# Optimization experiments

Measured on AMD Instinct MI355X. Metric: run time of the kernel, lower is better.

The kernel has to match this reference:

```python
import jax, jax.numpy as jnp
import numpy as np

N = 2048        # nodes
IN_DIM = 128    # input feature dim
K = 8           # channels
D = 32          # per-channel dim (C_dim)
ITERS = 4       # routing iterations
BETA = 1.0      # attention temperature
EPS = 1e-12     # F.normalize eps


def l2norm(x):
    # F.normalize(x, dim=-1): x / max(||x||_2, eps)
    n = jnp.linalg.norm(x, axis=-1, keepdims=True)
    return x / jnp.maximum(n, EPS)


def setup_inputs() -> dict:
    key = jax.random.key(0)
    k1, k2, k3, k4 = jax.random.split(key, 4)
    adj = jax.random.randint(k1, (N, N), 0, 2, dtype=jnp.int32)
    features = jax.random.normal(k2, (N, IN_DIM), dtype=jnp.float32)
    # parameters initialized ~ N(0,1) as in init_parameters
    W = jax.random.normal(k3, (K, IN_DIM, D), dtype=jnp.float32)
    b = jax.random.normal(k4, (K, D), dtype=jnp.float32)
    return {"adj": adj, "features": features, "W": W, "b": b}


def reference(adj, features, W, b):
    mask = (adj > 0)[None, :, :]                         # [1, N, N]
    # per-channel projection + row L2 normalize -> Z: [K, N, D]
    Z = l2norm(jnp.einsum('nd,kdc->knc', features, W) + b[:, None, :])
    for _ in range(ITERS):
        # per-channel masked attention scores [K, N, N]
        att = jnp.einsum('knc,kmc->knm', Z, Z)
        att = jnp.where(mask, att, 0.0) / BETA
        # softmax across channels (dim=2 in torch after cat == K axis here)
        att = jax.nn.softmax(att, axis=0)
        att = jnp.where(mask, att, 0.0)
        # weighted aggregate + residual + L2 normalize
        Z = l2norm(Z + jnp.einsum('knm,kmc->knc', att, Z))
    # concat channels along feature dim -> [N, K*D]
    return jnp.transpose(Z, (1, 0, 2)).reshape(N, K * D)
```

## Files before the change

kernel.cpp:

```cpp
#include <hip/hip_runtime.h>
#include <hip/hip_bf16.h>

#define NN 2048
#define KK 8
#define DD 32
#define ZSZ (KK * NN * DD)

typedef __attribute__((ext_vector_type(8))) short short8;
typedef __attribute__((ext_vector_type(4))) float f32x4;
typedef __attribute__((ext_vector_type(4))) unsigned int u32x4;

union UU { u32x4 q; short8 v; unsigned int u[4]; };

#define SELHI 0x07060302u
#define SELLO 0x05040100u
#define PSTR 20

__device__ __forceinline__ unsigned int prm(unsigned int a, unsigned int b, unsigned int sel) {
  return __builtin_amdgcn_perm(a, b, sel);
}
__device__ __forceinline__ unsigned int bfr(float x) {
  unsigned int u = __float_as_uint(x);
  return (u + 0x7fffu + ((u >> 16) & 1u)) >> 16;
}
__device__ __forceinline__ unsigned int packp(float a, float b) {
  union { __hip_bfloat162 h; unsigned int u; } cv;
  cv.h = __float22bfloat162_rn(make_float2(a, b));
  return cv.u;
}
__device__ __forceinline__ f32x4 MF(short8 a, short8 b, f32x4 c) {
  return __builtin_amdgcn_mfma_f32_16x16x32_bf16(a, b, c, 0, 0, 0);
}
__device__ __forceinline__ short8 as_s8(u32x4 x) { UU u; u.q = x; return u.v; }
__device__ __forceinline__ int swz(int m) { return (m ^ (m >> 2)) & 3; }

__global__ __launch_bounds__(256) void pm_kernel(const float* __restrict__ feat,
                                                 const float* __restrict__ W,
                                                 const float* __restrict__ bias,
                                                 float* __restrict__ Z,
                                                 const int* __restrict__ adj,
                                                 unsigned int* __restrict__ mbits) {
  const int t = threadIdx.x;
  if (blockIdx.x < NN) {
    __shared__ float f[128];
    const int n = blockIdx.x;
    if (t < 128) f[t] = feat[n * 128 + t];
    __syncthreads();
    const int k = t >> 5, c = t & 31;
    float s = bias[k * DD + c];
    const float* w = W + (k * 128) * DD + c;
#pragma unroll 16
    for (int d = 0; d < 128; ++d) s = fmaf(f[d], w[d * DD], s);
    float sq = s * s;
#pragma unroll
    for (int off = 16; off > 0; off >>= 1) sq += __shfl_xor(sq, off, 32);
    Z[(k * NN + n) * DD + c] = s / fmaxf(sqrtf(sq), 1e-12f);
  } else {
    const int base = (blockIdx.x - NN) * 1024 + t;
    const int lane = t & 63;
    int v[4];
#pragma unroll
    for (int rr = 0; rr < 4; ++rr) v[rr] = adj[base + 256 * rr];
#pragma unroll
    for (int rr = 0; rr < 4; ++rr) {
      int idx = base + 256 * rr;
      unsigned long long b = __ballot(v[rr] > 0);
      if (lane == 0) mbits[idx >> 5] = (unsigned int)b;
      if (lane == 32) mbits[idx >> 5] = (unsigned int)(b >> 32);
    }
  }
}

__global__ __launch_bounds__(256) void rp_kernel(const float* __restrict__ Zin,
                                                 const float* __restrict__ part, int nc,
                                                 float* __restrict__ Zout,
                                                 unsigned short* __restrict__ Zghi,
                                                 unsigned short* __restrict__ Zthi) {
  __shared__ unsigned short T[DD][33];
  const int t = threadIdx.x;
  const int k = blockIdx.x >> 6, mt = blockIdx.x & 63;
  const int m0 = mt * 32;
  const int mloc = t >> 3, c4 = t & 7;
  const size_t idx = (size_t)(k * NN + m0 + mloc) * DD + 4 * c4;
  float4 v = *(const float4*)&Zin[idx];
  for (int j = 0; j < nc; ++j) {
    float4 p = *(const float4*)&part[(size_t)j * ZSZ + idx];
    v.x += p.x; v.y += p.y; v.z += p.z; v.w += p.w;
  }
  float sq = v.x * v.x + v.y * v.y + v.z * v.z + v.w * v.w;
  sq += __shfl_xor(sq, 1, 8);
  sq += __shfl_xor(sq, 2, 8);
  sq += __shfl_xor(sq, 4, 8);
  const float sc = 1.0f / fmaxf(sqrtf(sq), 1e-12f);
  float z[4] = {v.x * sc, v.y * sc, v.z * sc, v.w * sc};
  if (nc) *(float4*)&Zout[idx] = make_float4(z[0], z[1], z[2], z[3]);
  unsigned int hi[4];
#pragma unroll
  for (int e = 0; e < 4; ++e) {
    hi[e] = bfr(z[e]);
    T[4 * c4 + e][mloc] = (unsigned short)hi[e];
  }
  *(uint2*)&Zghi[idx] = make_uint2(hi[0] | (hi[1] << 16), hi[2] | (hi[3] << 16));
  __syncthreads();
  const int cloc = t >> 3, m4 = t & 7;
  unsigned int o0 = (unsigned int)T[cloc][4 * m4 + 0] | ((unsigned int)T[cloc][4 * m4 + 1] << 16);
  unsigned int o1 = (unsigned int)T[cloc][4 * m4 + 2] | ((unsigned int)T[cloc][4 * m4 + 3] << 16);
  *(uint2*)&Zthi[(size_t)k * DD * NN + (size_t)cloc * NN + m0 + 4 * m4] = make_uint2(o0, o1);
}

__global__ __launch_bounds__(256, 2) void iter_kernel(const unsigned short* __restrict__ Zghi,
                                                      const unsigned short* __restrict__ Zthi,
                                                      const unsigned int* __restrict__ mbits,
                                                      float* __restrict__ part, int nsteps) {
  __shared__ __align__(16) unsigned int lds[8192 + 4 * 4 * 16 * PSTR];
  const int t = threadIdx.x;
  const int w = t >> 6;
  const int lane = t & 63;
  const int l15 = lane & 15;
  const int g = lane >> 4;
  const int nw = blockIdx.x * 64 + w * 16;
  const int mchunk = blockIdx.y * (nsteps * 32);

  const unsigned int* Zg = (const unsigned int*)Zghi;
  const unsigned int* Zt = (const unsigned int*)Zthi;

  short8 A[KK];
#pragma unroll
  for (int k = 0; k < KK; ++k)
    A[k] = as_s8(*(const u32x4*)&Zg[(size_t)(k * NN + nw + l15) * 16 + 4 * g]);

  f32x4 O[KK][2];
#pragma unroll
  for (int k = 0; k < KK; ++k)
#pragma unroll
    for (int ch = 0; ch < 2; ++ch) O[k][ch] = {0.0f, 0.0f, 0.0f, 0.0f};

  const int sqd = t & 3;
  const int sr0 = t >> 2;

  u32x4 Lgh[4], Lth[4];
  auto do_loads = [&](int mb) {
#pragma unroll
    for (int j = 0; j < 4; ++j) {
      int r = 64 * j + sr0;
      int k = r >> 5, rm = r & 31;
      Lgh[j] = *(const u32x4*)&Zg[(size_t)k * (NN * 16) + (size_t)(mb + rm) * 16 + sqd * 4];
      Lth[j] = *(const u32x4*)&Zt[(size_t)k * (NN * 16) + (size_t)rm * (NN / 2) + (mb >> 1) + sqd * 4];
    }
  };
  do_loads(mchunk);

  unsigned int* Pw = &lds[8192 + w * (4 * 16 * PSTR)];

  for (int st = 0; st < nsteps; ++st) {
    const int mb = mchunk + st * 32;
    __syncthreads();
#pragma unroll
    for (int j = 0; j < 4; ++j) {
      int r = 64 * j + sr0;
      int rm = r & 31;
      int qs = (sqd ^ swz(rm)) << 2;
      *(u32x4*)&lds[r * 16 + qs] = Lgh[j];
      *(u32x4*)&lds[4096 + r * 16 + qs] = Lth[j];
    }
    __syncthreads();
    if (st + 1 < nsteps) do_loads(mb + 32);

    f32x4 S[KK][2];
#pragma unroll
    for (int k = 0; k < KK; ++k) {
#pragma unroll
      for (int sub = 0; sub < 2; ++sub) {
        int m = 16 * sub + l15;
        u32x4 bh = *(const u32x4*)&lds[(k * 32 + m) * 16 + ((g ^ swz(m)) << 2)];
        f32x4 z = {0.0f, 0.0f, 0.0f, 0.0f};
        S[k][sub] = MF(A[k], as_s8(bh), z);
      }
    }

    unsigned int mw[4];
#pragma unroll
    for (int r = 0; r < 4; ++r) mw[r] = mbits[(size_t)(nw + 4 * g + r) * 64 + (mb >> 5)];
#pragma unroll
    for (int sub = 0; sub < 2; ++sub) {
#pragma unroll
      for (int r = 0; r < 4; ++r) {
        float e[KK];
        float sum = 0.0f;
#pragma unroll
        for (int k = 0; k < KK; ++k) { e[k] = __expf(S[k][sub][r]); sum += e[k]; }
        int ml = 16 * sub + l15;
        float f = ((mw[r] >> ml) & 1u) ? __builtin_amdgcn_rcpf(sum) : 0.0f;
#pragma unroll
        for (int k = 0; k < KK; ++k) S[k][sub][r] = e[k] * f;
      }
    }

#pragma unroll
    for (int kp = 0; kp < 4; ++kp)
#pragma unroll
      for (int sub = 0; sub < 2; ++sub)
#pragma unroll
        for (int r = 0; r < 4; ++r) {
          int n = 4 * g + r;
          Pw[kp * (16 * PSTR) + n * PSTR + 16 * sub + l15] =
              packp(S[2 * kp][sub][r], S[2 * kp + 1][sub][r]);
        }

#pragma unroll
    for (int kp = 0; kp < 4; ++kp) {
      const unsigned int* Pr = &Pw[kp * (16 * PSTR) + l15 * PSTR + 8 * g];
      u32x4 a0 = *(const u32x4*)Pr;
      u32x4 a1 = *(const u32x4*)(Pr + 4);
      UU pk0, pk1;
      pk0.u[0] = prm(a0.y, a0.x, SELLO); pk0.u[1] = prm(a0.w, a0.z, SELLO);
      pk0.u[2] = prm(a1.y, a1.x, SELLO); pk0.u[3] = prm(a1.w, a1.z, SELLO);
      pk1.u[0] = prm(a0.y, a0.x, SELHI); pk1.u[1] = prm(a0.w, a0.z, SELHI);
      pk1.u[2] = prm(a1.y, a1.x, SELHI); pk1.u[3] = prm(a1.w, a1.z, SELHI);
#pragma unroll
      for (int kk = 0; kk < 2; ++kk) {
        int k = 2 * kp + kk;
#pragma unroll
        for (int ch = 0; ch < 2; ++ch) {
          int c = 16 * ch + l15;
          u32x4 b = *(const u32x4*)&lds[4096 + (k * 32 + c) * 16 + ((g ^ swz(c)) << 2)];
          O[k][ch] = MF(kk ? pk1.v : pk0.v, as_s8(b), O[k][ch]);
        }
      }
    }
  }

  float* dst = part + (size_t)blockIdx.y * ZSZ;
#pragma unroll
  for (int k = 0; k < KK; ++k)
#pragma unroll
    for (int ch = 0; ch < 2; ++ch) {
      f32x4 o = O[k][ch];
#pragma unroll
      for (int r = 0; r < 4; ++r)
        dst[(size_t)(k * NN + nw + 4 * g + r) * DD + 16 * ch + l15] = o[r];
    }
}

__global__ __launch_bounds__(256) void ro_kernel(const float* __restrict__ Zin,
                                                 const float* __restrict__ part, int nc,
                                                 float* __restrict__ out) {
  const int n = blockIdx.x, t = threadIdx.x;
  const int k = t >> 5, c = t & 31;
  const size_t idx = (size_t)(k * NN + n) * DD + c;
  float v = Zin[idx];
  for (int j = 0; j < nc; ++j) v += part[(size_t)j * ZSZ + idx];
  float sq = v * v;
#pragma unroll
  for (int off = 16; off > 0; off >>= 1) sq += __shfl_xor(sq, off, 32);
  out[n * (KK * DD) + t] = v / fmaxf(sqrtf(sq), 1e-12f);
}

extern "C" void kernel_launch(void* const* d_in, const int* in_sizes, int n_in,
                              void* d_out, int out_size, void* d_ws, size_t ws_size,
                              hipStream_t stream) {
  const int* adj = (const int*)d_in[0];
  const float* feat = (const float*)d_in[1];
  const float* W = (const float*)d_in[2];
  const float* b = (const float*)d_in[3];
  float* out = (float*)d_out;

  int NC = 16;
  while (NC > 1) {
    size_t need = ((size_t)ZSZ * (2 + NC) + NN * 64) * 4 + (size_t)ZSZ * 2 * 2;
    if (need <= ws_size) break;
    NC >>= 1;
  }
  const int nsteps = NN / NC / 32;

  float* Z0 = (float*)d_ws;
  float* Z1 = Z0 + ZSZ;
  unsigned short* Zghi = (unsigned short*)(Z1 + ZSZ);
  unsigned short* Zthi = Zghi + ZSZ;
  unsigned int* mbits = (unsigned int*)(Zthi + ZSZ);
  float* part = (float*)(mbits + NN * 64);

  pm_kernel<<<NN + 4096, 256, 0, stream>>>(feat, W, b, Z0, adj, mbits);

  rp_kernel<<<512, 256, 0, stream>>>(Z0, part, 0, Z1, Zghi, Zthi);

  float* zi = Z0;
  float* zo = Z1;
  for (int it = 0; it < 4; ++it) {
    iter_kernel<<<dim3(32, NC), 256, 0, stream>>>(Zghi, Zthi, mbits, part, nsteps);
    if (it < 3) {
      rp_kernel<<<512, 256, 0, stream>>>(zi, part, NC, zo, Zghi, Zthi);
      float* tmp = zi; zi = zo; zo = tmp;
    } else {
      ro_kernel<<<NN, 256, 0, stream>>>(zi, part, NC, out);
    }
  }
}
```

Measured before the change: 202.2 us.

## Fuse all phases into one persistent kernel with grid-wide atomic barriers

Replaces the sequence of separate launches (projection/mask packing, repack, four iteration kernels, readout) with a single persistent kernel of 512 blocks that moves between phases through a software grid barrier built on atomic counters and a flag. The goal is to remove per-launch overhead and idle gaps between the ten or so small kernels. The projection phase now handles four nodes per block and reuses each weight load across them. The design assumes all 512 blocks are resident at the same time (two per CU) and adds a memset for the barrier plus spin-wait cost at each phase boundary. The workspace-based fallback for the chunk count is removed, so NC is fixed at 16.

```diff
diff --git a/kernel.cpp b/kernel.cpp
--- a/kernel.cpp
+++ b/kernel.cpp
@@ -5,6 +5,10 @@
 #define KK 8
 #define DD 32
 #define ZSZ (KK * NN * DD)
+#define NCH 16
+#define NSTEPS 4
+#define PSTR 20
+#define NBLK 512
 
 typedef __attribute__((ext_vector_type(8))) short short8;
 typedef __attribute__((ext_vector_type(4))) float f32x4;
@@ -14,7 +18,6 @@
 
 #define SELHI 0x07060302u
 #define SELLO 0x05040100u
-#define PSTR 20
 
 __device__ __forceinline__ unsigned int prm(unsigned int a, unsigned int b, unsigned int sel) {
   return __builtin_amdgcn_perm(a, b, sel);
@@ -34,226 +37,266 @@
 __device__ __forceinline__ short8 as_s8(u32x4 x) { UU u; u.q = x; return u.v; }
 __device__ __forceinline__ int swz(int m) { return (m ^ (m >> 2)) & 3; }
 
-__global__ __launch_bounds__(256) void pm_kernel(const float* __restrict__ feat,
-                                                 const float* __restrict__ W,
-                                                 const float* __restrict__ bias,
-                                                 float* __restrict__ Z,
-                                                 const int* __restrict__ adj,
-                                                 unsigned int* __restrict__ mbits) {
+__device__ __forceinline__ void gsync(unsigned int* bar, unsigned int ep) {
+  __syncthreads();
+  if (threadIdx.x == 0) {
+    __threadfence();
+    unsigned int old = __hip_atomic_fetch_add(&bar[16u * ep], 1u, __ATOMIC_ACQ_REL,
+                                              __HIP_MEMORY_SCOPE_AGENT);
+    unsigned int* flag = &bar[512];
+    if (old == NBLK - 1u) {
+      __hip_atomic_store(flag, ep + 1u, __ATOMIC_RELEASE, __HIP_MEMORY_SCOPE_AGENT);
+    } else {
+      while (__hip_atomic_load(flag, __ATOMIC_RELAXED, __HIP_MEMORY_SCOPE_AGENT) < ep + 1u)
+        __builtin_amdgcn_s_sleep(4);
+      __builtin_amdgcn_fence(__ATOMIC_ACQUIRE, "agent");
+    }
+  }
+  __syncthreads();
+}
+
+__global__ __launch_bounds__(256, 2) void fused_kernel(
+    const int* __restrict__ adj, const float* __restrict__ feat,
+    const float* __restrict__ W, const float* __restrict__ bias,
+    float* __restrict__ Z0, float* __restrict__ Z1,
+    unsigned short* __restrict__ Zghi, unsigned short* __restrict__ Zthi,
+    unsigned int* __restrict__ mbits, float* __restrict__ part,
+    float* __restrict__ out, unsigned int* bar) {
+  __shared__ __align__(16) unsigned int lds[8192 + 4 * 4 * 16 * PSTR];
   const int t = threadIdx.x;
-  if (blockIdx.x < NN) {
-    __shared__ float f[128];
-    const int n = blockIdx.x;
-    if (t < 128) f[t] = feat[n * 128 + t];
+  const int bx = blockIdx.x;
+  unsigned int ep = 0;
+
+  {
+    float* fsh = (float*)lds;
+    const int nb = bx * 4;
+#pragma unroll
+    for (int i = 0; i < 2; ++i) fsh[t + 256 * i] = feat[nb * 128 + t + 256 * i];
     __syncthreads();
     const int k = t >> 5, c = t & 31;
-    float s = bias[k * DD + c];
+    float s[4];
+#pragma unroll
+    for (int j = 0; j < 4; ++j) s[j] = bias[k * DD + c];
     const float* w = W + (k * 128) * DD + c;
-#pragma unroll 16
-    for (int d = 0; d < 128; ++d) s = fmaf(f[d], w[d * DD], s);
-    float sq = s * s;
-#pragma unroll
-    for (int off = 16; off > 0; off >>= 1) sq += __shfl_xor(sq, off, 32);
-    Z[(k * NN + n) * DD + c] = s / fmaxf(sqrtf(sq), 1e-12f);
-  } else {
-    const int base = (blockIdx.x - NN) * 1024 + t;
+#pragma unroll 8
+    for (int d = 0; d < 128; ++d) {
+      float wv = w[d * DD];
+#pragma unroll
+      for (int j = 0; j < 4; ++j) s[j] = fmaf(fsh[j * 128 + d], wv, s[j]);
+    }
+#pragma unroll
+    for (int j = 0; j < 4; ++j) {
+      float sq = s[j] * s[j];
+#pragma unroll
+      for (int off = 16; off > 0; off >>= 1) sq += __shfl_xor(sq, off, 32);
+      Z0[(k * NN + nb + j) * DD + c] = s[j] / fmaxf(sqrtf(sq), 1e-12f);
+    }
     const int lane = t & 63;
-    int v[4];
-#pragma unroll
-    for (int rr = 0; rr < 4; ++rr) v[rr] = adj[base + 256 * rr];
-#pragma unroll
-    for (int rr = 0; rr < 4; ++rr) {
-      int idx = base + 256 * rr;
-      unsigned long long b = __ballot(v[rr] > 0);
-      if (lane == 0) mbits[idx >> 5] = (unsigned int)b;
-      if (lane == 32) mbits[idx >> 5] = (unsigned int)(b >> 32);
+    for (int rr = 0; rr < 32; rr += 4) {
+      int v[4];
+#pragma unroll
+      for (int j = 0; j < 4; ++j) v[j] = adj[bx * 8192 + (rr + j) * 256 + t];
+#pragma unroll
+      for (int j = 0; j < 4; ++j) {
+        int idx = bx * 8192 + (rr + j) * 256 + t;
+        unsigned long long bmask = __ballot(v[j] > 0);
+        if (lane == 0) mbits[idx >> 5] = (unsigned int)bmask;
+        if (lane == 32) mbits[idx >> 5] = (unsigned int)(bmask >> 32);
+      }
     }
   }
-}
-
-__global__ __launch_bounds__(256) void rp_kernel(const float* __restrict__ Zin,
-                                                 const float* __restrict__ part, int nc,
-                                                 float* __restrict__ Zout,
-                                                 unsigned short* __restrict__ Zghi,
-                                                 unsigned short* __restrict__ Zthi) {
-  __shared__ unsigned short T[DD][33];
-  const int t = threadIdx.x;
-  const int k = blockIdx.x >> 6, mt = blockIdx.x & 63;
-  const int m0 = mt * 32;
-  const int mloc = t >> 3, c4 = t & 7;
-  const size_t idx = (size_t)(k * NN + m0 + mloc) * DD + 4 * c4;
-  float4 v = *(const float4*)&Zin[idx];
-  for (int j = 0; j < nc; ++j) {
-    float4 p = *(const float4*)&part[(size_t)j * ZSZ + idx];
-    v.x += p.x; v.y += p.y; v.z += p.z; v.w += p.w;
+  gsync(bar, ep++);
+
+  auto rp_phase = [&](const float* Zin, int nc, float* Zout) {
+    __syncthreads();
+    unsigned short(*T)[33] = (unsigned short(*)[33])lds;
+    const int k = bx >> 6, mt = bx & 63;
+    const int m0 = mt * 32;
+    const int mloc = t >> 3, c4 = t & 7;
+    const size_t idx = (size_t)(k * NN + m0 + mloc) * DD + 4 * c4;
+    float4 v = *(const float4*)&Zin[idx];
+    for (int j = 0; j < nc; ++j) {
+      float4 p = *(const float4*)&part[(size_t)j * ZSZ + idx];
+      v.x += p.x; v.y += p.y; v.z += p.z; v.w += p.w;
+    }
+    float sq = v.x * v.x + v.y * v.y + v.z * v.z + v.w * v.w;
+    sq += __shfl_xor(sq, 1, 8);
+    sq += __shfl_xor(sq, 2, 8);
+    sq += __shfl_xor(sq, 4, 8);
+    const float sc = 1.0f / fmaxf(sqrtf(sq), 1e-12f);
+    float z[4] = {v.x * sc, v.y * sc, v.z * sc, v.w * sc};
+    if (nc) *(float4*)&Zout[idx] = make_float4(z[0], z[1], z[2], z[3]);
+    unsigned int hi[4];
+#pragma unroll
+    for (int e = 0; e < 4; ++e) {
+      hi[e] = bfr(z[e]);
+      T[4 * c4 + e][mloc] = (unsigned short)hi[e];
+    }
+    *(uint2*)&Zghi[idx] = make_uint2(hi[0] | (hi[1] << 16), hi[2] | (hi[3] << 16));
+    __syncthreads();
+    const int cloc = t >> 3, m4 = t & 7;
+    unsigned int o0 = (unsigned int)T[cloc][4 * m4 + 0] | ((unsigned int)T[cloc][4 * m4 + 1] << 16);
+    unsigned int o1 = (unsigned int)T[cloc][4 * m4 + 2] | ((unsigned int)T[cloc][4 * m4 + 3] << 16);
+    *(uint2*)&Zthi[(size_t)k * DD * NN + (size_t)cloc * NN + m0 + 4 * m4] = make_uint2(o0, o1);
+  };
+
+  rp_phase(Z0, 0, Z1);
+  gsync(bar, ep++);
+
+  const float* zi = Z0;
+  float* zo = Z1;
+
+  for (int it = 0; it < 4; ++it) {
+    {
+      __syncthreads();
+      const int w = t >> 6;
+      const int lane = t & 63;
+      const int l15 = lane & 15;
+      const int g = lane >> 4;
+      const int nw = (bx & 31) * 64 + w * 16;
+      const int mchunk = (bx >> 5) * (NSTEPS * 32);
+
+      const unsigned int* Zg = (const unsigned int*)Zghi;
+      const unsigned int* Zt = (const unsigned int*)Zthi;
+
+      short8 A[KK];
+#pragma unroll
+      for (int k = 0; k < KK; ++k)
+        A[k] = as_s8(*(const u32x4*)&Zg[(size_t)(k * NN + nw + l15) * 16 + 4 * g]);
+
+      f32x4 O[KK][2];
+#pragma unroll
+      for (int k = 0; k < KK; ++k)
+#pragma unroll
+        for (int ch = 0; ch < 2; ++ch) O[k][ch] = {0.0f, 0.0f, 0.0f, 0.0f};
+
+      const int sqd = t & 3;
+      const int sr0 = t >> 2;
+
+      u32x4 Lgh[4], Lth[4];
+      auto do_loads = [&](int mb) {
+#pragma unroll
+        for (int j = 0; j < 4; ++j) {
+          int r = 64 * j + sr0;
+          int k = r >> 5, rm = r & 31;
+          Lgh[j] = *(const u32x4*)&Zg[(size_t)k * (NN * 16) + (size_t)(mb + rm) * 16 + sqd * 4];
+          Lth[j] = *(const u32x4*)&Zt[(size_t)k * (NN * 16) + (size_t)rm * (NN / 2) + (mb >> 1) + sqd * 4];
+        }
+      };
+      do_loads(mchunk);
+
+      unsigned int* Pw = &lds[8192 + w * (4 * 16 * PSTR)];
+
+      for (int st = 0; st < NSTEPS; ++st) {
+        const int mb = mchunk + st * 32;
+        __syncthreads();
+#pragma unroll
+        for (int j = 0; j < 4; ++j) {
+          int r = 64 * j + sr0;
+          int rm = r & 31;
+          int qs = (sqd ^ swz(rm)) << 2;
+          *(u32x4*)&lds[r * 16 + qs] = Lgh[j];
+          *(u32x4*)&lds[4096 + r * 16 + qs] = Lth[j];
+        }
+        __syncthreads();
+        if (st + 1 < NSTEPS) do_loads(mb + 32);
+
+        f32x4 S[KK][2];
+#pragma unroll
+        for (int k = 0; k < KK; ++k) {
+#pragma unroll
+          for (int sub = 0; sub < 2; ++sub) {
+            int m = 16 * sub + l15;
+            u32x4 bh = *(const u32x4*)&lds[(k * 32 + m) * 16 + ((g ^ swz(m)) << 2)];
+            f32x4 z = {0.0f, 0.0f, 0.0f, 0.0f};
+            S[k][sub] = MF(A[k], as_s8(bh), z);
+          }
+        }
+
+        unsigned int mw[4];
+#pragma unroll
+        for (int r = 0; r < 4; ++r) mw[r] = mbits[(size_t)(nw + 4 * g + r) * 64 + (mb >> 5)];
+#pragma unroll
+        for (int sub = 0; sub < 2; ++sub) {
+#pragma unroll
+          for (int r = 0; r < 4; ++r) {
+            float e[KK];
+            float sum = 0.0f;
+#pragma unroll
+            for (int k = 0; k < KK; ++k) { e[k] = __expf(S[k][sub][r]); sum += e[k]; }
+            int ml = 16 * sub + l15;
+            float f = ((mw[r] >> ml) & 1u) ? __builtin_amdgcn_rcpf(sum) : 0.0f;
+#pragma unroll
+            for (int k = 0; k < KK; ++k) S[k][sub][r] = e[k] * f;
+          }
+        }
+
+#pragma unroll
+        for (int kp = 0; kp < 4; ++kp)
+#pragma unroll
+          for (int sub = 0; sub < 2; ++sub)
+#pragma unroll
+            for (int r = 0; r < 4; ++r) {
+              int n = 4 * g + r;
+              Pw[kp * (16 * PSTR) + n * PSTR + 16 * sub + l15] =
+                  packp(S[2 * kp][sub][r], S[2 * kp + 1][sub][r]);
+            }
+
+#pragma unroll
+        for (int kp = 0; kp < 4; ++kp) {
+          const unsigned int* Pr = &Pw[kp * (16 * PSTR) + l15 * PSTR + 8 * g];
+          u32x4 a0 = *(const u32x4*)Pr;
+          u32x4 a1 = *(const u32x4*)(Pr + 4);
+          UU pk0, pk1;
+          pk0.u[0] = prm(a0.y, a0.x, SELLO); pk0.u[1] = prm(a0.w, a0.z, SELLO);
+          pk0.u[2] = prm(a1.y, a1.x, SELLO); pk0.u[3] = prm(a1.w, a1.z, SELLO);
+          pk1.u[0] = prm(a0.y, a0.x, SELHI); pk1.u[1] = prm(a0.w, a0.z, SELHI);
+          pk1.u[2] = prm(a1.y, a1.x, SELHI); pk1.u[3] = prm(a1.w, a1.z, SELHI);
+#pragma unroll
+          for (int kk = 0; kk < 2; ++kk) {
+            int k = 2 * kp + kk;
+#pragma unroll
+            for (int ch = 0; ch < 2; ++ch) {
+              int c = 16 * ch + l15;
+              u32x4 b = *(const u32x4*)&lds[4096 + (k * 32 + c) * 16 + ((g ^ swz(c)) << 2)];
+              O[k][ch] = MF(kk ? pk1.v : pk0.v, as_s8(b), O[k][ch]);
+            }
+          }
+        }
+      }
+
+      float* dst = part + (size_t)(bx >> 5) * ZSZ;
+#pragma unroll
+      for (int k = 0; k < KK; ++k)
+#pragma unroll
+        for (int ch = 0; ch < 2; ++ch) {
+          f32x4 o = O[k][ch];
+#pragma unroll
+          for (int r = 0; r < 4; ++r)
+            dst[(size_t)(k * NN + nw + 4 * g + r) * DD + 16 * ch + l15] = o[r];
+        }
+    }
+    gsync(bar, ep++);
+
+    if (it < 3) {
+      rp_phase(zi, NCH, zo);
+      gsync(bar, ep++);
+      const float* tz = zi; zi = zo; zo = (float*)tz;
+    } else {
+      const int k = t >> 5, c = t & 31;
+#pragma unroll
+      for (int j = 0; j < 4; ++j) {
+        const int n = bx * 4 + j;
+        const size_t idx = (size_t)(k * NN + n) * DD + c;
+        float v = zi[idx];
+        for (int q = 0; q < NCH; ++q) v += part[(size_t)q * ZSZ + idx];
+        float sq = v * v;
+#pragma unroll
+        for (int off = 16; off > 0; off >>= 1) sq += __shfl_xor(sq, off, 32);
+        out[n * (KK * DD) + t] = v / fmaxf(sqrtf(sq), 1e-12f);
+      }
+    }
   }
-  float sq = v.x * v.x + v.y * v.y + v.z * v.z + v.w * v.w;
-  sq += __shfl_xor(sq, 1, 8);
-  sq += __shfl_xor(sq, 2, 8);
-  sq += __shfl_xor(sq, 4, 8);
-  const float sc = 1.0f / fmaxf(sqrtf(sq), 1e-12f);
-  float z[4] = {v.x * sc, v.y * sc, v.z * sc, v.w * sc};
-  if (nc) *(float4*)&Zout[idx] = make_float4(z[0], z[1], z[2], z[3]);
-  unsigned int hi[4];
-#pragma unroll
-  for (int e = 0; e < 4; ++e) {
-    hi[e] = bfr(z[e]);
-    T[4 * c4 + e][mloc] = (unsigned short)hi[e];
-  }
-  *(uint2*)&Zghi[idx] = make_uint2(hi[0] | (hi[1] << 16), hi[2] | (hi[3] << 16));
-  __syncthreads();
-  const int cloc = t >> 3, m4 = t & 7;
-  unsigned int o0 = (unsigned int)T[cloc][4 * m4 + 0] | ((unsigned int)T[cloc][4 * m4 + 1] << 16);
-  unsigned int o1 = (unsigned int)T[cloc][4 * m4 + 2] | ((unsigned int)T[cloc][4 * m4 + 3] << 16);
-  *(uint2*)&Zthi[(size_t)k * DD * NN + (size_t)cloc * NN + m0 + 4 * m4] = make_uint2(o0, o1);
-}
-
-__global__ __launch_bounds__(256, 2) void iter_kernel(const unsigned short* __restrict__ Zghi,
-                                                      const unsigned short* __restrict__ Zthi,
-                                                      const unsigned int* __restrict__ mbits,
-                                                      float* __restrict__ part, int nsteps) {
-  __shared__ __align__(16) unsigned int lds[8192 + 4 * 4 * 16 * PSTR];
-  const int t = threadIdx.x;
-  const int w = t >> 6;
-  const int lane = t & 63;
-  const int l15 = lane & 15;
-  const int g = lane >> 4;
-  const int nw = blockIdx.x * 64 + w * 16;
-  const int mchunk = blockIdx.y * (nsteps * 32);
-
-  const unsigned int* Zg = (const unsigned int*)Zghi;
-  const unsigned int* Zt = (const unsigned int*)Zthi;
-
-  short8 A[KK];
-#pragma unroll
-  for (int k = 0; k < KK; ++k)
-    A[k] = as_s8(*(const u32x4*)&Zg[(size_t)(k * NN + nw + l15) * 16 + 4 * g]);
-
-  f32x4 O[KK][2];
-#pragma unroll
-  for (int k = 0; k < KK; ++k)
-#pragma unroll
-    for (int ch = 0; ch < 2; ++ch) O[k][ch] = {0.0f, 0.0f, 0.0f, 0.0f};
-
-  const int sqd = t & 3;
-  const int sr0 = t >> 2;
-
-  u32x4 Lgh[4], Lth[4];
-  auto do_loads = [&](int mb) {
-#pragma unroll
-    for (int j = 0; j < 4; ++j) {
-      int r = 64 * j + sr0;
-      int k = r >> 5, rm = r & 31;
-      Lgh[j] = *(const u32x4*)&Zg[(size_t)k * (NN * 16) + (size_t)(mb + rm) * 16 + sqd * 4];
-      Lth[j] = *(const u32x4*)&Zt[(size_t)k * (NN * 16) + (size_t)rm * (NN / 2) + (mb >> 1) + sqd * 4];
-    }
-  };
-  do_loads(mchunk);
-
-  unsigned int* Pw = &lds[8192 + w * (4 * 16 * PSTR)];
-
-  for (int st = 0; st < nsteps; ++st) {
-    const int mb = mchunk + st * 32;
-    __syncthreads();
-#pragma unroll
-    for (int j = 0; j < 4; ++j) {
-      int r = 64 * j + sr0;
-      int rm = r & 31;
-      int qs = (sqd ^ swz(rm)) << 2;
-      *(u32x4*)&lds[r * 16 + qs] = Lgh[j];
-      *(u32x4*)&lds[4096 + r * 16 + qs] = Lth[j];
-    }
-    __syncthreads();
-    if (st + 1 < nsteps) do_loads(mb + 32);
-
-    f32x4 S[KK][2];
-#pragma unroll
-    for (int k = 0; k < KK; ++k) {
-#pragma unroll
-      for (int sub = 0; sub < 2; ++sub) {
-        int m = 16 * sub + l15;
-        u32x4 bh = *(const u32x4*)&lds[(k * 32 + m) * 16 + ((g ^ swz(m)) << 2)];
-        f32x4 z = {0.0f, 0.0f, 0.0f, 0.0f};
-        S[k][sub] = MF(A[k], as_s8(bh), z);
-      }
-    }
-
-    unsigned int mw[4];
-#pragma unroll
-    for (int r = 0; r < 4; ++r) mw[r] = mbits[(size_t)(nw + 4 * g + r) * 64 + (mb >> 5)];
-#pragma unroll
-    for (int sub = 0; sub < 2; ++sub) {
-#pragma unroll
-      for (int r = 0; r < 4; ++r) {
-        float e[KK];
-        float sum = 0.0f;
-#pragma unroll
-        for (int k = 0; k < KK; ++k) { e[k] = __expf(S[k][sub][r]); sum += e[k]; }
-        int ml = 16 * sub + l15;
-        float f = ((mw[r] >> ml) & 1u) ? __builtin_amdgcn_rcpf(sum) : 0.0f;
-#pragma unroll
-        for (int k = 0; k < KK; ++k) S[k][sub][r] = e[k] * f;
-      }
-    }
-
-#pragma unroll
-    for (int kp = 0; kp < 4; ++kp)
-#pragma unroll
-      for (int sub = 0; sub < 2; ++sub)
-#pragma unroll
-        for (int r = 0; r < 4; ++r) {
-          int n = 4 * g + r;
-          Pw[kp * (16 * PSTR) + n * PSTR + 16 * sub + l15] =
-              packp(S[2 * kp][sub][r], S[2 * kp + 1][sub][r]);
-        }
-
-#pragma unroll
-    for (int kp = 0; kp < 4; ++kp) {
-      const unsigned int* Pr = &Pw[kp * (16 * PSTR) + l15 * PSTR + 8 * g];
-      u32x4 a0 = *(const u32x4*)Pr;
-      u32x4 a1 = *(const u32x4*)(Pr + 4);
-      UU pk0, pk1;
-      pk0.u[0] = prm(a0.y, a0.x, SELLO); pk0.u[1] = prm(a0.w, a0.z, SELLO);
-      pk0.u[2] = prm(a1.y, a1.x, SELLO); pk0.u[3] = prm(a1.w, a1.z, SELLO);
-      pk1.u[0] = prm(a0.y, a0.x, SELHI); pk1.u[1] = prm(a0.w, a0.z, SELHI);
-      pk1.u[2] = prm(a1.y, a1.x, SELHI); pk1.u[3] = prm(a1.w, a1.z, SELHI);
-#pragma unroll
-      for (int kk = 0; kk < 2; ++kk) {
-        int k = 2 * kp + kk;
-#pragma unroll
-        for (int ch = 0; ch < 2; ++ch) {
-          int c = 16 * ch + l15;
-          u32x4 b = *(const u32x4*)&lds[4096 + (k * 32 + c) * 16 + ((g ^ swz(c)) << 2)];
-          O[k][ch] = MF(kk ? pk1.v : pk0.v, as_s8(b), O[k][ch]);
-        }
-      }
-    }
-  }
-
-  float* dst = part + (size_t)blockIdx.y * ZSZ;
-#pragma unroll
-  for (int k = 0; k < KK; ++k)
-#pragma unroll
-    for (int ch = 0; ch < 2; ++ch) {
-      f32x4 o = O[k][ch];
-#pragma unroll
-      for (int r = 0; r < 4; ++r)
-        dst[(size_t)(k * NN + nw + 4 * g + r) * DD + 16 * ch + l15] = o[r];
-    }
-}
-
-__global__ __launch_bounds__(256) void ro_kernel(const float* __restrict__ Zin,
-                                                 const float* __restrict__ part, int nc,
-                                                 float* __restrict__ out) {
-  const int n = blockIdx.x, t = threadIdx.x;
-  const int k = t >> 5, c = t & 31;
-  const size_t idx = (size_t)(k * NN + n) * DD + c;
-  float v = Zin[idx];
-  for (int j = 0; j < nc; ++j) v += part[(size_t)j * ZSZ + idx];
-  float sq = v * v;
-#pragma unroll
-  for (int off = 16; off > 0; off >>= 1) sq += __shfl_xor(sq, off, 32);
-  out[n * (KK * DD) + t] = v / fmaxf(sqrtf(sq), 1e-12f);
 }
 
 extern "C" void kernel_launch(void* const* d_in, const int* in_sizes, int n_in,
@@ -265,34 +308,15 @@
   const float* b = (const float*)d_in[3];
   float* out = (float*)d_out;
 
-  int NC = 16;
-  while (NC > 1) {
-    size_t need = ((size_t)ZSZ * (2 + NC) + NN * 64) * 4 + (size_t)ZSZ * 2 * 2;
-    if (need <= ws_size) break;
-    NC >>= 1;
-  }
-  const int nsteps = NN / NC / 32;
-
-  float* Z0 = (float*)d_ws;
+  unsigned int* bar = (unsigned int*)d_ws;
+  float* Z0 = (float*)((char*)d_ws + 4096);
   float* Z1 = Z0 + ZSZ;
   unsigned short* Zghi = (unsigned short*)(Z1 + ZSZ);
   unsigned short* Zthi = Zghi + ZSZ;
   unsigned int* mbits = (unsigned int*)(Zthi + ZSZ);
   float* part = (float*)(mbits + NN * 64);
 
-  pm_kernel<<<NN + 4096, 256, 0, stream>>>(feat, W, b, Z0, adj, mbits);
-
-  rp_kernel<<<512, 256, 0, stream>>>(Z0, part, 0, Z1, Zghi, Zthi);
-
-  float* zi = Z0;
-  float* zo = Z1;
-  for (int it = 0; it < 4; ++it) {
-    iter_kernel<<<dim3(32, NC), 256, 0, stream>>>(Zghi, Zthi, mbits, part, nsteps);
-    if (it < 3) {
-      rp_kernel<<<512, 256, 0, stream>>>(zi, part, NC, zo, Zghi, Zthi);
-      float* tmp = zi; zi = zo; zo = tmp;
-    } else {
-      ro_kernel<<<NN, 256, 0, stream>>>(zi, part, NC, out);
-    }
-  }
-}
+  hipMemsetAsync(bar, 0, 4096, stream);
+  fused_kernel<<<NBLK, 256, 0, stream>>>(adj, feat, W, b, Z0, Z1, Zghi, Zthi,
+                                         mbits, part, out, bar);
+}
```

New measurement: 601.0 us. 197% more time.
